# Optimization experiments

Measured on AMD Instinct MI355X. Metric: run time of the kernel, lower is better.

The kernel has to match this reference:

```python
import jax, jax.numpy as jnp
import numpy as np

GROUPS = 32
EPS = 1e-5


def group_norm(x, gamma, beta):
    B, C, D, H, W = x.shape
    xr = x.reshape(B, GROUPS, C // GROUPS, D, H, W)
    mean = xr.mean(axis=(2, 3, 4, 5), keepdims=True)
    var = xr.var(axis=(2, 3, 4, 5), keepdims=True)
    xn = (xr - mean) * jax.lax.rsqrt(var + EPS)
    xn = xn.reshape(B, C, D, H, W)
    return xn * gamma[None, :, None, None, None] + beta[None, :, None, None, None]


def conv1x1(h, w, b):
    # 1x1x1 Conv3d == channel matmul. w: [O, C], b: [O]
    return jnp.einsum('oc,bcdhw->bodhw', w, h) + b[None, :, None, None, None]


def setup_inputs() -> dict:
    key = jax.random.key(0)
    ks = jax.random.split(key, 10)
    B, C, D, H, W = 2, 128, 16, 16, 16
    x = jax.random.normal(ks[0], (B, C, D, H, W), dtype=jnp.float32)
    gn_w = jnp.ones((C,), dtype=jnp.float32)
    gn_b = jnp.zeros((C,), dtype=jnp.float32)
    # xavier_uniform for [C, C, 1, 1, 1] conv: fan_in = fan_out = C
    lim = float(np.sqrt(6.0 / (C + C)))
    wq = jax.random.uniform(ks[1], (C, C), jnp.float32, -lim, lim)
    wk = jax.random.uniform(ks[2], (C, C), jnp.float32, -lim, lim)
    wv = jax.random.uniform(ks[3], (C, C), jnp.float32, -lim, lim)
    wp = jax.random.uniform(ks[4], (C, C), jnp.float32, -lim, lim) * 1e-05
    bq = jnp.zeros((C,), jnp.float32)
    bk = jnp.zeros((C,), jnp.float32)
    bv = jnp.zeros((C,), jnp.float32)
    bp = jnp.zeros((C,), jnp.float32)
    return {"x": x, "gn_w": gn_w, "gn_b": gn_b, "wq": wq, "bq": bq,
            "wk": wk, "bk": bk, "wv": wv, "bv": bv, "wp": wp, "bp": bp}


def reference(x, gn_w, gn_b, wq, bq, wk, bk, wv, bv, wp, bp):
    B, C, D, H, W = x.shape
    N = D * H * W
    h = group_norm(x, gn_w, gn_b)
    q = conv1x1(h, wq, bq)
    k = conv1x1(h, wk, bk)
    v = conv1x1(h, wv, bv)
    q = q.transpose(0, 2, 3, 4, 1).reshape(B, N, C)   # [B, N, C]
    k = k.reshape(B, C, N)                            # [B, C, N]
    v = v.transpose(0, 2, 3, 4, 1).reshape(B, N, C)   # [B, N, C]
    w = jnp.einsum('bnc,bcm->bnm', q, k) * (C ** -0.5)  # [B, N, N]
    w = jax.nn.softmax(w, axis=-1)
    h = jnp.einsum('bnm,bmc->bnc', w, v)              # [B, N, C]
    h = h.reshape(B, D, H, W, C).transpose(0, 4, 1, 2, 3)
    h = conv1x1(h, wp, bp)
    return x + h
```

## Files before the change

kernel.cpp:

```cpp
#include <hip/hip_runtime.h>
#include <math.h>

#define CC 128
#define NN 4096
#define BB 2
#define NGROUPS 32
#define CPG 4
#define GSIZE (CPG*NN)
#define KSPLIT 2

typedef __attribute__((ext_vector_type(8))) __bf16 bf16x8;
typedef __attribute__((ext_vector_type(4))) float floatx4;

__device__ __forceinline__ unsigned short f2bf(float f) {
  union { float f; unsigned u; } v; v.f = f;
  unsigned r = v.u + 0x7fff + ((v.u >> 16) & 1);
  return (unsigned short)(r >> 16);
}
__device__ __forceinline__ float bf2f(unsigned short u) {
  return __uint_as_float(((unsigned)u) << 16);
}


__global__ void gn_stats_kernel(const float* __restrict__ x, float2* __restrict__ stats,
                                const float* __restrict__ wq, const float* __restrict__ wk,
                                const float* __restrict__ wv, const float* __restrict__ wp,
                                unsigned short* __restrict__ wqb, unsigned short* __restrict__ wkb,
                                unsigned short* __restrict__ wvb, unsigned short* __restrict__ wpb) {
  int t = threadIdx.x;
  if (blockIdx.x < 256) {
    int bid = blockIdx.x;
    const float4* base = (const float4*)(x + (size_t)bid * 4096);
    float4 v = base[t];
    float s  = v.x + v.y + v.z + v.w;
    float ss = v.x*v.x + v.y*v.y + v.z*v.z + v.w*v.w;
    #pragma unroll
    for (int off = 1; off < 64; off <<= 1) {
      s  += __shfl_xor(s, off);
      ss += __shfl_xor(ss, off);
    }
    __shared__ float sred[4], ssred[4];
    if ((t & 63) == 0) { sred[t >> 6] = s; ssred[t >> 6] = ss; }
    __syncthreads();
    if (t == 0)
      stats[bid] = make_float2(sred[0]+sred[1]+sred[2]+sred[3],
                               ssred[0]+ssred[1]+ssred[2]+ssred[3]);
  } else {
    const float sc = 0.08838834764831845f;
    int i = (blockIdx.x - 256) * 256 + t;
    int id = i >> 12, local = i & 4095;
    const float* src = id==0 ? wq : id==1 ? wk : id==2 ? wv : wp;
    unsigned short* dst = id==0 ? wqb : id==1 ? wkb : id==2 ? wvb : wpb;
    float s = (id == 0) ? sc : 1.0f;
    float4 v = ((const float4*)src)[local];
    unsigned p0 = (unsigned)f2bf(v.x*s) | ((unsigned)f2bf(v.y*s) << 16);
    unsigned p1 = (unsigned)f2bf(v.z*s) | ((unsigned)f2bf(v.w*s) << 16);
    ((uint2*)dst)[local] = make_uint2(p0, p1);
  }
}

__global__ __launch_bounds__(256, 2) void qkv_kernel(
    const float* __restrict__ x, const float2* __restrict__ stats,
    const float* __restrict__ gamma, const float* __restrict__ beta,
    const unsigned short* __restrict__ wqb, const unsigned short* __restrict__ wkb,
    const unsigned short* __restrict__ wvb,
    const float* __restrict__ bq, const float* __restrict__ bk, const float* __restrict__ bv,
    unsigned short* __restrict__ q, unsigned short* __restrict__ k, unsigned short* __restrict__ v) {
  int z = blockIdx.z, b = blockIdx.y, n0 = blockIdx.x * 32;
  const unsigned short* wsel = z==0 ? wqb : z==1 ? wkb : wvb;
  const float* bias          = z==0 ? bq  : z==1 ? bk  : bv;
  float bscale               = z==0 ? 0.08838834764831845f : 1.0f;
  unsigned short* outp       = z==0 ? q   : z==1 ? k   : v;
  __shared__ unsigned short hs[32][130];
  __shared__ unsigned short vs[32][136];
  __shared__ float gm[NGROUPS], gr[NGROUPS], aa[CC], ab[CC];
  int t = threadIdx.x;
  if (t < NGROUPS) {
    float su = 0.f, ssq = 0.f;
    #pragma unroll
    for (int j = 0; j < 4; j++) {
      float2 p = stats[(b*NGROUPS + t)*4 + j];
      su += p.x; ssq += p.y;
    }
    float mean = su * (1.0f/GSIZE);
    float var  = ssq * (1.0f/GSIZE) - mean*mean;
    gm[t] = mean;
    gr[t] = rsqrtf(var + 1e-5f);
  }
  __syncthreads();
  if (t < CC) {
    int g = t >> 2;
    float a = gr[g] * gamma[t];
    aa[t] = a;
    ab[t] = beta[t] - gm[g] * a;
  }
  __syncthreads();
  #pragma unroll
  for (int j = 0; j < 16; j++) {
    int idx = j*256 + t;
    int c = idx >> 5, n = idx & 31;
    float xv = x[((size_t)b*CC + c)*NN + n0 + n];
    hs[n][c] = f2bf(aa[c]*xv + ab[c]);
  }
  __syncthreads();
  int w = t >> 6, lane = t & 63, quad = lane >> 4, c = lane & 15;
  int o0 = w * 32;
  floatx4 acc[2][2];
  #pragma unroll
  for (int rt = 0; rt < 2; rt++)
    #pragma unroll
    for (int ct = 0; ct < 2; ct++) acc[rt][ct] = (floatx4){0.f,0.f,0.f,0.f};
  #pragma unroll
  for (int ks = 0; ks < 4; ks++) {
    bf16x8 af[2];
    af[0] = *(const bf16x8*)&hs[c     ][ks*32 + quad*8];
    af[1] = *(const bf16x8*)&hs[16 + c][ks*32 + quad*8];
    #pragma unroll
    for (int ct = 0; ct < 2; ct++) {
      bf16x8 bfr = *(const bf16x8*)(wsel + (size_t)(o0 + ct*16 + c)*CC + ks*32 + quad*8);
      acc[0][ct] = __builtin_amdgcn_mfma_f32_16x16x32_bf16(af[0], bfr, acc[0][ct], 0, 0, 0);
      acc[1][ct] = __builtin_amdgcn_mfma_f32_16x16x32_bf16(af[1], bfr, acc[1][ct], 0, 0, 0);
    }
  }
  if (z < 2) {
    size_t base = (size_t)b*NN*CC + ((size_t)(n0 >> 4))*2048 + w*512;
    #pragma unroll
    for (int ct = 0; ct < 2; ct++) {
      float bi = bias[o0 + ct*16 + c] * bscale;
      #pragma unroll
      for (int rt = 0; rt < 2; rt++)
        #pragma unroll
        for (int r = 0; r < 4; r++)
          outp[base + rt*2048 + (quad*4 + r)*32 + ct*16 + c] = f2bf(acc[rt][ct][r] + bi);
    }
  } else {
    #pragma unroll
    for (int ct = 0; ct < 2; ct++) {
      float bi = bias[o0 + ct*16 + c];
      #pragma unroll
      for (int rt = 0; rt < 2; rt++)
        #pragma unroll
        for (int r = 0; r < 4; r++)
          vs[rt*16 + quad*4 + r][o0 + ct*16 + c] = f2bf(acc[rt][ct][r] + bi);
    }
    __syncthreads();
    int ct = t >> 5;
    int rem = t & 31;
    int c16 = rem >> 1;
    int m0 = (rem & 1) * 16;
    int ch = ct*16 + c16;
    unsigned pk[8];
    #pragma unroll
    for (int j2 = 0; j2 < 8; j2++) {
      unsigned lo = vs[m0 + j2*2    ][ch];
      unsigned hi = vs[m0 + j2*2 + 1][ch];
      pk[j2] = lo | (hi << 16);
    }
    uint4* dst = (uint4*)(outp + (size_t)b*NN*CC + ((size_t)(n0 >> 5))*4096 + ct*512 + c16*32 + m0);
    dst[0] = make_uint4(pk[0], pk[1], pk[2], pk[3]);
    dst[1] = make_uint4(pk[4], pk[5], pk[6], pk[7]);
  }
}

__global__ __launch_bounds__(256, 2) void attn_kernel(
    const unsigned short* __restrict__ qm,
    const unsigned short* __restrict__ km,
    const unsigned short* __restrict__ vm,
    unsigned short* __restrict__ Opart,
    float* __restrict__ lpart) {
  int b    = blockIdx.z;
  int kh   = blockIdx.y;
  int row0 = blockIdx.x * 32;
  int t    = threadIdx.x;
  int w    = t >> 6, lane = t & 63, quad = lane >> 4, c = lane & 15;

  __shared__ unsigned short shmem[4][32][132];
  __shared__ float lred[4][32];
  unsigned short (*Pl)[72] = (unsigned short (*)[72])&shmem[w][0][0];

  int fragoff = c*32 + quad*8;

  bf16x8 qa[2][4];
  const unsigned short* qbase = qm + (size_t)b*NN*CC + ((size_t)(row0 >> 4))*2048;
  #pragma unroll
  for (int rt = 0; rt < 2; rt++)
    #pragma unroll
    for (int ks = 0; ks < 4; ks++)
      qa[rt][ks] = *(const bf16x8*)(qbase + rt*2048 + ks*512 + fragoff);

  floatx4 O[2][8];
  #pragma unroll
  for (int rt = 0; rt < 2; rt++)
    #pragma unroll
    for (int ct = 0; ct < 8; ct++) O[rt][ct] = (floatx4){0.f,0.f,0.f,0.f};
  float lsum[2][4];
  #pragma unroll
  for (int rt = 0; rt < 2; rt++)
    #pragma unroll
    for (int r = 0; r < 4; r++) lsum[rt][r] = 0.f;

  const unsigned short* kb0 = km + (size_t)b*NN*CC;
  const unsigned short* vb0 = vm + (size_t)b*NN*CC;
  const unsigned short* ktbase = kb0 + ((size_t)(kh*128 + w*4))*2048;
  const unsigned short* vtbase = vb0 + ((size_t)(kh*64  + w*2))*4096;

  const int ITERS = NN/KSPLIT/256;

  bf16x8 kf[4][4];
  #pragma unroll
  for (int ks = 0; ks < 4; ks++)
    #pragma unroll
    for (int ct = 0; ct < 4; ct++)
      kf[ks][ct] = *(const bf16x8*)(ktbase + ct*2048 + ks*512 + fragoff);

  for (int it = 0; it < ITERS; it++) {
    const unsigned short* vt  = vtbase + (size_t)it*32768;
    const unsigned short* ktn = ktbase + (size_t)((it+1 < ITERS) ? it+1 : it)*32768;
    floatx4 S[2][4];
    #pragma unroll
    for (int rt = 0; rt < 2; rt++)
      #pragma unroll
      for (int ct = 0; ct < 4; ct++) S[rt][ct] = (floatx4){0.f,0.f,0.f,0.f};
    #pragma unroll
    for (int ks = 0; ks < 4; ks++) {
      #pragma unroll
      for (int ct = 0; ct < 4; ct++) {
        S[0][ct] = __builtin_amdgcn_mfma_f32_16x16x32_bf16(qa[0][ks], kf[ks][ct], S[0][ct], 0, 0, 0);
        S[1][ct] = __builtin_amdgcn_mfma_f32_16x16x32_bf16(qa[1][ks], kf[ks][ct], S[1][ct], 0, 0, 0);
      }
    }
    bf16x8 kfn[4][4];
    #pragma unroll
    for (int ks = 0; ks < 4; ks++)
      #pragma unroll
      for (int ct = 0; ct < 4; ct++)
        kfn[ks][ct] = *(const bf16x8*)(ktn + ct*2048 + ks*512 + fragoff);
    #pragma unroll
    for (int rt = 0; rt < 2; rt++) {
      #pragma unroll
      for (int ct = 0; ct < 4; ct++) {
        float e0 = __expf(S[rt][ct][0]);
        float e1 = __expf(S[rt][ct][1]);
        float e2 = __expf(S[rt][ct][2]);
        float e3 = __expf(S[rt][ct][3]);
        lsum[rt][0] += e0; lsum[rt][1] += e1;
        lsum[rt][2] += e2; lsum[rt][3] += e3;
        bool odd = (c & 1);
        float s01 = odd ? e0 : e1;
        float g01 = __shfl_xor(s01, 1);
        unsigned lo0 = __float_as_uint(odd ? g01 : e0);
        unsigned hi0 = __float_as_uint(odd ? e1 : g01);
        unsigned p0 = (hi0 & 0xffff0000u) | (lo0 >> 16);
        float s23 = odd ? e2 : e3;
        float g23 = __shfl_xor(s23, 1);
        unsigned lo1 = __float_as_uint(odd ? g23 : e2);
        unsigned hi1 = __float_as_uint(odd ? e3 : g23);
        unsigned p1 = (hi1 & 0xffff0000u) | (lo1 >> 16);
        int colpair = ct*16 + (c & ~1);
        int rowA = rt*16 + quad*4 + (odd ? 1 : 0);
        int rowB = rt*16 + quad*4 + (odd ? 3 : 2);
        *(unsigned*)&Pl[rowA][colpair] = p0;
        *(unsigned*)&Pl[rowB][colpair] = p1;
      }
    }
    #pragma unroll
    for (int ks2 = 0; ks2 < 2; ks2++) {
      bf16x8 pa0 = *(const bf16x8*)(&Pl[c     ][ks2*32 + quad*8]);
      bf16x8 pa1 = *(const bf16x8*)(&Pl[16 + c][ks2*32 + quad*8]);
      #pragma unroll
      for (int ct = 0; ct < 8; ct++) {
        bf16x8 vf = *(const bf16x8*)(vt + ks2*4096 + ct*512 + fragoff);
        O[0][ct] = __builtin_amdgcn_mfma_f32_16x16x32_bf16(pa0, vf, O[0][ct], 0, 0, 0);
        O[1][ct] = __builtin_amdgcn_mfma_f32_16x16x32_bf16(pa1, vf, O[1][ct], 0, 0, 0);
      }
    }
    #pragma unroll
    for (int ks = 0; ks < 4; ks++)
      #pragma unroll
      for (int ct = 0; ct < 4; ct++)
        kf[ks][ct] = kfn[ks][ct];
  }

  #pragma unroll
  for (int rt = 0; rt < 2; rt++)
    #pragma unroll
    for (int r = 0; r < 4; r++) {
      float vsum = lsum[rt][r];
      vsum += __shfl_xor(vsum, 1);
      vsum += __shfl_xor(vsum, 2);
      vsum += __shfl_xor(vsum, 4);
      vsum += __shfl_xor(vsum, 8);
      if (c == 0) lred[w][rt*16 + quad*4 + r] = vsum;
    }
  __syncthreads();
  #pragma unroll
  for (int rt = 0; rt < 2; rt++)
    #pragma unroll
    for (int ct = 0; ct < 8; ct++)
      #pragma unroll
      for (int r = 0; r < 4; r++)
        shmem[w][rt*16 + quad*4 + r][ct*16 + c] = f2bf(O[rt][ct][r]);
  __syncthreads();
  size_t pbase = (size_t)(kh*BB + b)*NN + row0;
  if (t < 32)
    lpart[pbase + t] = lred[0][t] + lred[1][t] + lred[2][t] + lred[3][t];
  int rr = t >> 3, c0 = (t & 7) * 16;
  unsigned pk[8];
  #pragma unroll
  for (int j2 = 0; j2 < 8; j2++) {
    int cc0 = c0 + j2*2;
    float v0 = bf2f(shmem[0][rr][cc0])   + bf2f(shmem[1][rr][cc0])
             + bf2f(shmem[2][rr][cc0])   + bf2f(shmem[3][rr][cc0]);
    float v1 = bf2f(shmem[0][rr][cc0+1]) + bf2f(shmem[1][rr][cc0+1])
             + bf2f(shmem[2][rr][cc0+1]) + bf2f(shmem[3][rr][cc0+1]);
    pk[j2] = (unsigned)f2bf(v0) | ((unsigned)f2bf(v1) << 16);
  }
  uint4* od = (uint4*)(Opart + (pbase + rr)*CC + c0);
  od[0] = make_uint4(pk[0], pk[1], pk[2], pk[3]);
  od[1] = make_uint4(pk[4], pk[5], pk[6], pk[7]);
}

__global__ __launch_bounds__(256, 2) void combine_kernel(
    const unsigned short* __restrict__ Opart, const float* __restrict__ lpart,
    const unsigned short* __restrict__ wpb, const float* __restrict__ bp,
    const float* __restrict__ x, float* __restrict__ out) {
  int b = blockIdx.y, n0 = blockIdx.x * 32;
  int t = threadIdx.x;
  __shared__ unsigned short hs[32][130];
  __shared__ float ps[32][132];
  __shared__ float linv[32];
  if (t < 32) {
    float l = 0.f;
    #pragma unroll
    for (int kh = 0; kh < KSPLIT; kh++)
      l += lpart[((size_t)(kh*BB + b))*NN + n0 + t];
    linv[t] = 1.f / l;
  }
  __syncthreads();
  #pragma unroll
  for (int j = 0; j < 16; j++) {
    int idx = j*256 + t;
    int n = idx >> 7, c2 = idx & 127;
    float o = 0.f;
    #pragma unroll
    for (int kh = 0; kh < KSPLIT; kh++)
      o += bf2f(Opart[((size_t)(kh*BB + b)*NN + n0 + n)*CC + c2]);
    hs[n][c2] = f2bf(o * linv[n]);
  }
  __syncthreads();
  int w = t >> 6, lane = t & 63, quad = lane >> 4, c = lane & 15;
  int o0 = w * 32;
  floatx4 acc[2][2];
  #pragma unroll
  for (int rt = 0; rt < 2; rt++)
    #pragma unroll
    for (int ct = 0; ct < 2; ct++) acc[rt][ct] = (floatx4){0.f,0.f,0.f,0.f};
  #pragma unroll
  for (int ks = 0; ks < 4; ks++) {
    bf16x8 af[2];
    af[0] = *(const bf16x8*)&hs[c     ][ks*32 + quad*8];
    af[1] = *(const bf16x8*)&hs[16 + c][ks*32 + quad*8];
    #pragma unroll
    for (int ct = 0; ct < 2; ct++) {
      bf16x8 bfr = *(const bf16x8*)(wpb + (size_t)(o0 + ct*16 + c)*CC + ks*32 + quad*8);
      acc[0][ct] = __builtin_amdgcn_mfma_f32_16x16x32_bf16(af[0], bfr, acc[0][ct], 0, 0, 0);
      acc[1][ct] = __builtin_amdgcn_mfma_f32_16x16x32_bf16(af[1], bfr, acc[1][ct], 0, 0, 0);
    }
  }
  #pragma unroll
  for (int rt = 0; rt < 2; rt++)
    #pragma unroll
    for (int ct = 0; ct < 2; ct++)
      #pragma unroll
      for (int r = 0; r < 4; r++)
        ps[rt*16 + quad*4 + r][o0 + ct*16 + c] = acc[rt][ct][r];
  __syncthreads();
  int o = t >> 1, nh = (t & 1) * 16;
  float bi = bp[o];
  const float* xr = x + ((size_t)b*CC + o)*NN + n0 + nh;
  float* orow = out + ((size_t)b*CC + o)*NN + n0 + nh;
  #pragma unroll
  for (int j4 = 0; j4 < 4; j4++) {
    float4 xv = ((const float4*)xr)[j4];
    float4 ov;
    ov.x = xv.x + ps[nh + j4*4 + 0][o] + bi;
    ov.y = xv.y + ps[nh + j4*4 + 1][o] + bi;
    ov.z = xv.z + ps[nh + j4*4 + 2][o] + bi;
    ov.w = xv.w + ps[nh + j4*4 + 3][o] + bi;
    ((float4*)orow)[j4] = ov;
  }
}

extern "C" void kernel_launch(void* const* d_in, const int* in_sizes, int n_in,
                              void* d_out, int out_size, void* d_ws, size_t ws_size,
                              hipStream_t stream) {
  const float* x    = (const float*)d_in[0];
  const float* gn_w = (const float*)d_in[1];
  const float* gn_b = (const float*)d_in[2];
  const float* wq   = (const float*)d_in[3];
  const float* bq   = (const float*)d_in[4];
  const float* wk   = (const float*)d_in[5];
  const float* bk   = (const float*)d_in[6];
  const float* wv   = (const float*)d_in[7];
  const float* bv   = (const float*)d_in[8];
  const float* wp   = (const float*)d_in[9];
  const float* bp   = (const float*)d_in[10];
  float* out = (float*)d_out;

  char* ws = (char*)d_ws;
  float2*         stats = (float2*)(ws);
  unsigned short* wqb   = (unsigned short*)(ws + 8192);
  unsigned short* wkb   = (unsigned short*)(ws + 8192 + 32768);
  unsigned short* wvb   = (unsigned short*)(ws + 8192 + 65536);
  unsigned short* wpb   = (unsigned short*)(ws + 8192 + 98304);
  unsigned short* qb    = (unsigned short*)(ws + 262144);
  unsigned short* kb    = (unsigned short*)(ws + 262144 + 2097152);
  unsigned short* vb    = (unsigned short*)(ws + 262144 + 2*2097152);
  unsigned short* Opart = (unsigned short*)(ws + 262144 + 3*2097152);
  float*          lpart = (float*)(ws + 262144 + 3*2097152 + 4194304);

  gn_stats_kernel<<<dim3(320), 256, 0, stream>>>(x, stats, wq, wk, wv, wp,
                                                 wqb, wkb, wvb, wpb);
  qkv_kernel     <<<dim3(NN/32, BB, 3), 256, 0, stream>>>(x, stats, gn_w, gn_b,
                                                          wqb, wkb, wvb, bq, bk, bv,
                                                          qb, kb, vb);
  attn_kernel    <<<dim3(NN/32, KSPLIT, BB), 256, 0, stream>>>(qb, kb, vb, Opart, lpart);
  combine_kernel <<<dim3(NN/32, BB), 256, 0, stream>>>(Opart, lpart, wpb, bp, x, out);
}
```

Baseline: 124.4 us.

## Share K/V tiles via LDS across waves and raise key split to eight

The attention kernel now has each wave own 32 distinct query rows (128 rows per block) and share K and V tiles staged into LDS with global_load_lds. Before, each wave read its own slice of keys straight from global memory and the partial outputs were reduced across waves. The key split rises from 2 to 8, so partial O/l buffers grow and combine sums more partials, now through vectorized uint4 loads. This trades global K/V traffic for LDS reads and two block barriers per iteration, with no double buffering of the staged tiles. It also writes more partial output to global memory.

```diff
diff --git a/kernel.cpp b/kernel.cpp
--- a/kernel.cpp
+++ b/kernel.cpp
@@ -7,7 +7,7 @@
 #define NGROUPS 32
 #define CPG 4
 #define GSIZE (CPG*NN)
-#define KSPLIT 2
+#define KSPLIT 8
 
 typedef __attribute__((ext_vector_type(8))) __bf16 bf16x8;
 typedef __attribute__((ext_vector_type(4))) float floatx4;
@@ -21,6 +21,18 @@
   return __uint_as_float(((unsigned)u) << 16);
 }
 
+
+__device__ __forceinline__ void stage_tile(const unsigned short* __restrict__ gtile,
+                                           unsigned short* ltile, int w, int lane) {
+  #pragma unroll
+  for (int j = 0; j < 4; j++) {
+    int off = (w*4 + j) * 512;
+    __builtin_amdgcn_global_load_lds(
+        (const __attribute__((address_space(1))) unsigned int*)(gtile + off + lane*8),
+        (__attribute__((address_space(3))) unsigned int*)(ltile + off),
+        16, 0, 0);
+  }
+}
 
 __global__ void gn_stats_kernel(const float* __restrict__ x, float2* __restrict__ stats,
                                 const float* __restrict__ wq, const float* __restrict__ wk,
@@ -170,18 +182,17 @@
     float* __restrict__ lpart) {
   int b    = blockIdx.z;
   int kh   = blockIdx.y;
-  int row0 = blockIdx.x * 32;
   int t    = threadIdx.x;
   int w    = t >> 6, lane = t & 63, quad = lane >> 4, c = lane & 15;
 
-  __shared__ unsigned short shmem[4][32][132];
-  __shared__ float lred[4][32];
-  unsigned short (*Pl)[72] = (unsigned short (*)[72])&shmem[w][0][0];
+  __shared__ unsigned short Kbuf[8192];
+  __shared__ unsigned short Vbuf[8192];
+  __shared__ unsigned short Pl[4][32][72];
 
   int fragoff = c*32 + quad*8;
 
   bf16x8 qa[2][4];
-  const unsigned short* qbase = qm + (size_t)b*NN*CC + ((size_t)(row0 >> 4))*2048;
+  const unsigned short* qbase = qm + (size_t)b*NN*CC + ((size_t)(blockIdx.x*8 + w*2))*2048;
   #pragma unroll
   for (int rt = 0; rt < 2; rt++)
     #pragma unroll
@@ -199,23 +210,16 @@
     #pragma unroll
     for (int r = 0; r < 4; r++) lsum[rt][r] = 0.f;
 
-  const unsigned short* kb0 = km + (size_t)b*NN*CC;
-  const unsigned short* vb0 = vm + (size_t)b*NN*CC;
-  const unsigned short* ktbase = kb0 + ((size_t)(kh*128 + w*4))*2048;
-  const unsigned short* vtbase = vb0 + ((size_t)(kh*64  + w*2))*4096;
-
-  const int ITERS = NN/KSPLIT/256;
-
-  bf16x8 kf[4][4];
-  #pragma unroll
-  for (int ks = 0; ks < 4; ks++)
-    #pragma unroll
-    for (int ct = 0; ct < 4; ct++)
-      kf[ks][ct] = *(const bf16x8*)(ktbase + ct*2048 + ks*512 + fragoff);
+  const unsigned short* kt0 = km + (size_t)b*NN*CC + (size_t)kh*32*2048;
+  const unsigned short* vt0 = vm + (size_t)b*NN*CC + (size_t)kh*16*4096;
+
+  const int ITERS = NN/KSPLIT/64;
+
+  stage_tile(kt0, Kbuf, w, lane);
+  stage_tile(vt0, Vbuf, w, lane);
+  __syncthreads();
 
   for (int it = 0; it < ITERS; it++) {
-    const unsigned short* vt  = vtbase + (size_t)it*32768;
-    const unsigned short* ktn = ktbase + (size_t)((it+1 < ITERS) ? it+1 : it)*32768;
     floatx4 S[2][4];
     #pragma unroll
     for (int rt = 0; rt < 2; rt++)
@@ -225,16 +229,11 @@
     for (int ks = 0; ks < 4; ks++) {
       #pragma unroll
       for (int ct = 0; ct < 4; ct++) {
-        S[0][ct] = __builtin_amdgcn_mfma_f32_16x16x32_bf16(qa[0][ks], kf[ks][ct], S[0][ct], 0, 0, 0);
-        S[1][ct] = __builtin_amdgcn_mfma_f32_16x16x32_bf16(qa[1][ks], kf[ks][ct], S[1][ct], 0, 0, 0);
+        bf16x8 kf = *(const bf16x8*)&Kbuf[ct*2048 + ks*512 + fragoff];
+        S[0][ct] = __builtin_amdgcn_mfma_f32_16x16x32_bf16(qa[0][ks], kf, S[0][ct], 0, 0, 0);
+        S[1][ct] = __builtin_amdgcn_mfma_f32_16x16x32_bf16(qa[1][ks], kf, S[1][ct], 0, 0, 0);
       }
     }
-    bf16x8 kfn[4][4];
-    #pragma unroll
-    for (int ks = 0; ks < 4; ks++)
-      #pragma unroll
-      for (int ct = 0; ct < 4; ct++)
-        kfn[ks][ct] = *(const bf16x8*)(ktn + ct*2048 + ks*512 + fragoff);
     #pragma unroll
     for (int rt = 0; rt < 2; rt++) {
       #pragma unroll
@@ -259,28 +258,28 @@
         int colpair = ct*16 + (c & ~1);
         int rowA = rt*16 + quad*4 + (odd ? 1 : 0);
         int rowB = rt*16 + quad*4 + (odd ? 3 : 2);
-        *(unsigned*)&Pl[rowA][colpair] = p0;
-        *(unsigned*)&Pl[rowB][colpair] = p1;
+        *(unsigned*)&Pl[w][rowA][colpair] = p0;
+        *(unsigned*)&Pl[w][rowB][colpair] = p1;
       }
     }
+    __syncthreads();
+    if (it+1 < ITERS) stage_tile(kt0 + (size_t)(it+1)*8192, Kbuf, w, lane);
     #pragma unroll
     for (int ks2 = 0; ks2 < 2; ks2++) {
-      bf16x8 pa0 = *(const bf16x8*)(&Pl[c     ][ks2*32 + quad*8]);
-      bf16x8 pa1 = *(const bf16x8*)(&Pl[16 + c][ks2*32 + quad*8]);
+      bf16x8 pa0 = *(const bf16x8*)(&Pl[w][c     ][ks2*32 + quad*8]);
+      bf16x8 pa1 = *(const bf16x8*)(&Pl[w][16 + c][ks2*32 + quad*8]);
       #pragma unroll
       for (int ct = 0; ct < 8; ct++) {
-        bf16x8 vf = *(const bf16x8*)(vt + ks2*4096 + ct*512 + fragoff);
+        bf16x8 vf = *(const bf16x8*)&Vbuf[ks2*4096 + ct*512 + fragoff];
         O[0][ct] = __builtin_amdgcn_mfma_f32_16x16x32_bf16(pa0, vf, O[0][ct], 0, 0, 0);
         O[1][ct] = __builtin_amdgcn_mfma_f32_16x16x32_bf16(pa1, vf, O[1][ct], 0, 0, 0);
       }
     }
-    #pragma unroll
-    for (int ks = 0; ks < 4; ks++)
-      #pragma unroll
-      for (int ct = 0; ct < 4; ct++)
-        kf[ks][ct] = kfn[ks][ct];
-  }
-
+    __syncthreads();
+    if (it+1 < ITERS) stage_tile(vt0 + (size_t)(it+1)*8192, Vbuf, w, lane);
+  }
+
+  size_t nbase = (size_t)(kh*BB + b)*NN + blockIdx.x*128 + w*32;
   #pragma unroll
   for (int rt = 0; rt < 2; rt++)
     #pragma unroll
@@ -290,34 +289,15 @@
       vsum += __shfl_xor(vsum, 2);
       vsum += __shfl_xor(vsum, 4);
       vsum += __shfl_xor(vsum, 8);
-      if (c == 0) lred[w][rt*16 + quad*4 + r] = vsum;
-    }
-  __syncthreads();
+      if (c == 0) lpart[nbase + rt*16 + quad*4 + r] = vsum;
+    }
   #pragma unroll
   for (int rt = 0; rt < 2; rt++)
     #pragma unroll
     for (int ct = 0; ct < 8; ct++)
       #pragma unroll
       for (int r = 0; r < 4; r++)
-        shmem[w][rt*16 + quad*4 + r][ct*16 + c] = f2bf(O[rt][ct][r]);
-  __syncthreads();
-  size_t pbase = (size_t)(kh*BB + b)*NN + row0;
-  if (t < 32)
-    lpart[pbase + t] = lred[0][t] + lred[1][t] + lred[2][t] + lred[3][t];
-  int rr = t >> 3, c0 = (t & 7) * 16;
-  unsigned pk[8];
-  #pragma unroll
-  for (int j2 = 0; j2 < 8; j2++) {
-    int cc0 = c0 + j2*2;
-    float v0 = bf2f(shmem[0][rr][cc0])   + bf2f(shmem[1][rr][cc0])
-             + bf2f(shmem[2][rr][cc0])   + bf2f(shmem[3][rr][cc0]);
-    float v1 = bf2f(shmem[0][rr][cc0+1]) + bf2f(shmem[1][rr][cc0+1])
-             + bf2f(shmem[2][rr][cc0+1]) + bf2f(shmem[3][rr][cc0+1]);
-    pk[j2] = (unsigned)f2bf(v0) | ((unsigned)f2bf(v1) << 16);
-  }
-  uint4* od = (uint4*)(Opart + (pbase + rr)*CC + c0);
-  od[0] = make_uint4(pk[0], pk[1], pk[2], pk[3]);
-  od[1] = make_uint4(pk[4], pk[5], pk[6], pk[7]);
+        Opart[(nbase + rt*16 + quad*4 + r)*CC + ct*16 + c] = f2bf(O[rt][ct][r]);
 }
 
 __global__ __launch_bounds__(256, 2) void combine_kernel(
@@ -337,15 +317,25 @@
     linv[t] = 1.f / l;
   }
   __syncthreads();
-  #pragma unroll
-  for (int j = 0; j < 16; j++) {
-    int idx = j*256 + t;
-    int n = idx >> 7, c2 = idx & 127;
-    float o = 0.f;
-    #pragma unroll
-    for (int kh = 0; kh < KSPLIT; kh++)
-      o += bf2f(Opart[((size_t)(kh*BB + b)*NN + n0 + n)*CC + c2]);
-    hs[n][c2] = f2bf(o * linv[n]);
+  {
+    int n = t >> 3, ch0 = (t & 7) * 16;
+    float acc[16];
+    #pragma unroll
+    for (int j = 0; j < 16; j++) acc[j] = 0.f;
+    #pragma unroll
+    for (int kh = 0; kh < KSPLIT; kh++) {
+      const uint4* src = (const uint4*)(Opart + ((size_t)(kh*BB + b)*NN + n0 + n)*CC + ch0);
+      uint4 a = src[0], bv = src[1];
+      unsigned uu[8] = {a.x, a.y, a.z, a.w, bv.x, bv.y, bv.z, bv.w};
+      #pragma unroll
+      for (int j = 0; j < 8; j++) {
+        acc[j*2    ] += bf2f((unsigned short)(uu[j] & 0xffff));
+        acc[j*2 + 1] += bf2f((unsigned short)(uu[j] >> 16));
+      }
+    }
+    float li = linv[n];
+    #pragma unroll
+    for (int j = 0; j < 16; j++) hs[n][ch0 + j] = f2bf(acc[j] * li);
   }
   __syncthreads();
   int w = t >> 6, lane = t & 63, quad = lane >> 4, c = lane & 15;
@@ -416,14 +406,14 @@
   unsigned short* qb    = (unsigned short*)(ws + 262144);
   unsigned short* kb    = (unsigned short*)(ws + 262144 + 2097152);
   unsigned short* vb    = (unsigned short*)(ws + 262144 + 2*2097152);
-  unsigned short* Opart = (unsigned short*)(ws + 262144 + 3*2097152);
-  float*          lpart = (float*)(ws + 262144 + 3*2097152 + 4194304);
+  unsigned short* Opart = (unsigned short*)(ws + 6553600);
+  float*          lpart = (float*)(ws + 6553600 + 16777216);
 
   gn_stats_kernel<<<dim3(320), 256, 0, stream>>>(x, stats, wq, wk, wv, wp,
                                                  wqb, wkb, wvb, wpb);
   qkv_kernel     <<<dim3(NN/32, BB, 3), 256, 0, stream>>>(x, stats, gn_w, gn_b,
                                                           wqb, wkb, wvb, bq, bk, bv,
                                                           qb, kb, vb);
-  attn_kernel    <<<dim3(NN/32, KSPLIT, BB), 256, 0, stream>>>(qb, kb, vb, Opart, lpart);
+  attn_kernel    <<<dim3(NN/128, KSPLIT, BB), 256, 0, stream>>>(qb, kb, vb, Opart, lpart);
   combine_kernel <<<dim3(NN/32, BB), 256, 0, stream>>>(Opart, lpart, wpb, bp, x, out);
 }
```

After: 120.7 us. 1.03x faster.
